# Kernel tuning notes

Hardware: AMD Instinct MI355X
Metric: run time of the kernel (lower is better)

Reference implementation:

```python
import jax, jax.numpy as jnp
import numpy as np


def setup_inputs() -> dict:
    key = jax.random.key(0)
    k1, k2 = jax.random.split(key)
    B, La, Lb, D = 32, 512, 512, 768
    a_bar = jax.random.normal(k1, (B, La, D), dtype=jnp.float32)
    b_bar = jax.random.normal(k2, (B, Lb, D), dtype=jnp.float32)
    return {"a_bar": a_bar, "b_bar": b_bar}


def reference(a_bar, b_bar):
    # e: [B, La, Lb] cross-attention scores
    e = jnp.einsum('bad,bcd->bac', a_bar, b_bar)
    # attend over b positions (softmax dim=2) -> aligned representation of a
    a_tilde = jnp.einsum('bac,bcd->bad', jax.nn.softmax(e, axis=2), b_bar)
    # attend over a positions (softmax dim=1), transpose, bmm with a_bar
    b_tilde = jnp.einsum('bac,bad->bcd', jax.nn.softmax(e, axis=1), a_bar)
    m_a = jnp.concatenate([a_bar, a_tilde, a_bar - a_tilde, a_bar * a_tilde], axis=-1)
    m_b = jnp.concatenate([b_bar, b_tilde, b_bar - b_tilde, b_bar * b_tilde], axis=-1)
    return (m_a, m_b)
```

## Files before the change

### kernel.cpp

```cpp
#include <hip/hip_runtime.h>
#include <hip/hip_bf16.h>
#include <math.h>

#define NB 32
#define LA 512
#define LB 512
#define DD 768

typedef __bf16 bf16x4 __attribute__((ext_vector_type(4)));
typedef __bf16 bf16x8 __attribute__((ext_vector_type(8)));
typedef float f32x4 __attribute__((ext_vector_type(4)));

__device__ __forceinline__ void gload_lds16(const void* g, void* l) {
  __builtin_amdgcn_global_load_lds(
      (const __attribute__((address_space(1))) unsigned int*)g,
      (__attribute__((address_space(3))) unsigned int*)l, 16, 0, 0);
}

__global__ __launch_bounds__(256) void convert_kernel(
    const float* __restrict__ A, const float* __restrict__ B,
    __bf16* __restrict__ Ah, __bf16* __restrict__ Al,
    __bf16* __restrict__ Bh, __bf16* __restrict__ Bl,
    __bf16* __restrict__ AhT, __bf16* __restrict__ BhT) {
  const int zb = blockIdx.z;
  const int b = zb & (NB - 1);
  const bool isB = zb >= NB;
  const float* src = (isB ? B : A) + (size_t)b * 512 * DD;
  __bf16* H = (isB ? Bh : Ah) + (size_t)b * 512 * DD;
  __bf16* L = (isB ? Bl : Al) + (size_t)b * 512 * DD;
  __bf16* T = (isB ? BhT : AhT) + (size_t)b * DD * 512;
  const int d0 = blockIdx.x * 64, i0 = blockIdx.y * 64;
  __shared__ __bf16 Tt[64][72];
  const int t = threadIdx.x;
  const int c4 = t & 15, r = t >> 4;
#pragma unroll
  for (int p = 0; p < 4; ++p) {
    const int i = i0 + r + p * 16;
    const float4 v = *(const float4*)(src + (size_t)i * DD + d0 + c4 * 4);
    float vv[4] = {v.x, v.y, v.z, v.w};
    bf16x4 h, l;
#pragma unroll
    for (int q = 0; q < 4; ++q) {
      h[q] = (__bf16)vv[q];
      l[q] = (__bf16)(vv[q] - (float)h[q]);
    }
    *(bf16x4*)(H + (size_t)i * DD + d0 + c4 * 4) = h;
    *(bf16x4*)(L + (size_t)i * DD + d0 + c4 * 4) = l;
#pragma unroll
    for (int q = 0; q < 4; ++q) Tt[c4 * 4 + q][r + p * 16] = h[q];
  }
  __syncthreads();
  const int cc = t & 7, rr = t >> 3;
#pragma unroll
  for (int p = 0; p < 2; ++p) {
    const int d = d0 + rr + p * 32;
    *(bf16x8*)(T + (size_t)d * 512 + i0 + cc * 8) =
        *(bf16x8*)&Tt[rr + p * 32][cc * 8];
  }
}

__global__ __launch_bounds__(256) void gemm_e_mfma(
    const __bf16* __restrict__ Ah, const __bf16* __restrict__ Al,
    const __bf16* __restrict__ Bh, const __bf16* __restrict__ Bl,
    float* __restrict__ E) {
  __shared__ __bf16 S[2][4][128][32];

  const int id = blockIdx.x;
  const int wg = (id & 7) * 64 + (id >> 3);
  const int b = wg >> 4, tl = wg & 15;
  const int i0 = (tl & 3) * 128, j0 = (tl >> 2) * 128;

  const __bf16* AhB = Ah + (size_t)b * LA * DD;
  const __bf16* AlB = Al + (size_t)b * LA * DD;
  const __bf16* BhB = Bh + (size_t)b * LB * DD;
  const __bf16* BlB = Bl + (size_t)b * LB * DD;
  float* Eb = E + (size_t)b * LA * LB;

  const int t = threadIdx.x;
  const int lane = t & 63, wave = t >> 6;
  const int wm = (wave >> 1) * 64, wn = (wave & 1) * 64;
  const int quad = lane >> 4, l16 = lane & 15;
  const int lrow = lane >> 2, lcol = (lane & 3) * 8;

  auto stage = [&](int buf, int k0) {
#pragma unroll
    for (int n = 0; n < 2; ++n) {
      const int c = n * 4 + wave;
      const int row = c * 16 + lrow;
      const size_t gA = (size_t)(i0 + row) * DD + k0 + lcol;
      const size_t gB = (size_t)(j0 + row) * DD + k0 + lcol;
      char* base = (char*)&S[buf][0][0][0];
      gload_lds16(AhB + gA, base + c * 1024);
      gload_lds16(AlB + gA, base + 8192 + c * 1024);
      gload_lds16(BhB + gB, base + 16384 + c * 1024);
      gload_lds16(BlB + gB, base + 24576 + c * 1024);
    }
  };

  f32x4 acc[4][4] = {};

  stage(0, 0);
  __syncthreads();
  int cur = 0;
  for (int k0 = 0; k0 < DD; k0 += 32) {
    if (k0 + 32 < DD) stage(cur ^ 1, k0 + 32);

    bf16x8 fah[4], fal[4], fbh[4], fbl[4];
#pragma unroll
    for (int f = 0; f < 4; ++f) {
      fah[f] = *(bf16x8*)&S[cur][0][wm + f * 16 + l16][quad * 8];
      fal[f] = *(bf16x8*)&S[cur][1][wm + f * 16 + l16][quad * 8];
      fbh[f] = *(bf16x8*)&S[cur][2][wn + f * 16 + l16][quad * 8];
      fbl[f] = *(bf16x8*)&S[cur][3][wn + f * 16 + l16][quad * 8];
    }
#pragma unroll
    for (int fm = 0; fm < 4; ++fm)
#pragma unroll
      for (int fn = 0; fn < 4; ++fn) {
        acc[fm][fn] = __builtin_amdgcn_mfma_f32_16x16x32_bf16(fah[fm], fbh[fn], acc[fm][fn], 0, 0, 0);
        acc[fm][fn] = __builtin_amdgcn_mfma_f32_16x16x32_bf16(fah[fm], fbl[fn], acc[fm][fn], 0, 0, 0);
        acc[fm][fn] = __builtin_amdgcn_mfma_f32_16x16x32_bf16(fal[fm], fbh[fn], acc[fm][fn], 0, 0, 0);
      }
    __syncthreads();
    cur ^= 1;
  }

#pragma unroll
  for (int fm = 0; fm < 4; ++fm)
#pragma unroll
    for (int r = 0; r < 4; ++r) {
      const int i = i0 + wm + fm * 16 + quad * 4 + r;
#pragma unroll
      for (int fn = 0; fn < 4; ++fn)
        Eb[(size_t)i * LB + j0 + wn + fn * 16 + l16] = acc[fm][fn][r];
    }
}

__global__ __launch_bounds__(256) void row_stats_kernel(
    const float* __restrict__ E, float* __restrict__ rmax,
    float* __restrict__ rsum) {
  const int wave = threadIdx.x >> 6;
  const int lane = threadIdx.x & 63;
  const int row = blockIdx.x * 4 + wave;
  const float* Er = E + (size_t)row * LB;
  float vals[8];
  float m = -INFINITY;
#pragma unroll
  for (int c = 0; c < 8; ++c) {
    vals[c] = Er[lane + c * 64];
    m = fmaxf(m, vals[c]);
  }
#pragma unroll
  for (int off = 32; off > 0; off >>= 1) m = fmaxf(m, __shfl_xor(m, off));
  float s = 0.f;
#pragma unroll
  for (int c = 0; c < 8; ++c) s += __expf(vals[c] - m);
#pragma unroll
  for (int off = 32; off > 0; off >>= 1) s += __shfl_xor(s, off);
  if (lane == 0) { rmax[row] = m; rsum[row] = s; }
}

__global__ __launch_bounds__(256) void col_partial(
    const float* __restrict__ E, float* __restrict__ pcm,
    float* __restrict__ pcs) {
  const int c = blockIdx.x * 256 + threadIdx.x;
  const int b = c >> 9, j = c & (LB - 1);
  const int i0 = blockIdx.y * 64;
  const float* Ep = E + ((size_t)b * LA + i0) * LB + j;
  float m = -INFINITY, s = 0.f;
#pragma unroll 4
  for (int i = 0; i < 64; ++i) {
    const float v = Ep[(size_t)i * LB];
    const float mn = fmaxf(m, v);
    s = s * __expf(m - mn) + __expf(v - mn);
    m = mn;
  }
  pcm[blockIdx.y * (NB * LB) + c] = m;
  pcs[blockIdx.y * (NB * LB) + c] = s;
}

__global__ __launch_bounds__(256) void col_combine(
    const float* __restrict__ pcm, const float* __restrict__ pcs,
    float* __restrict__ cmax, float* __restrict__ csum) {
  const int c = blockIdx.x * 256 + threadIdx.x;
  float m = -INFINITY, s = 0.f;
#pragma unroll
  for (int p = 0; p < 8; ++p) {
    const float mp = pcm[p * (NB * LB) + c];
    const float sp = pcs[p * (NB * LB) + c];
    const float mn = fmaxf(m, mp);
    s = s * __expf(m - mn) + sp * __expf(mp - mn);
    m = mn;
  }
  cmax[c] = m;
  csum[c] = s;
}

__global__ __launch_bounds__(256) void pconvert(
    const float* __restrict__ E, const float* __restrict__ rmax,
    const float* __restrict__ rsum, const float* __restrict__ cmax,
    const float* __restrict__ csum, __bf16* __restrict__ Pa,
    __bf16* __restrict__ PbT) {
  const int b = blockIdx.z;
  const int i0 = blockIdx.x * 128, j0 = blockIdx.y * 128;
  const float* Eb = E + (size_t)b * LA * LB;
  __shared__ __bf16 T[128][136];

  const int t = threadIdx.x;
  const int jr = t & 31, ir = t >> 5;
  const float4 cm4 = *(const float4*)&cmax[b * LB + j0 + jr * 4];
  const float4 cs4 = *(const float4*)&csum[b * LB + j0 + jr * 4];
  const float cmv[4] = {cm4.x, cm4.y, cm4.z, cm4.w};
  const float csv[4] = {1.f / cs4.x, 1.f / cs4.y, 1.f / cs4.z, 1.f / cs4.w};

#pragma unroll
  for (int p = 0; p < 16; ++p) {
    const int i = i0 + ir + p * 8;
    const float rm = rmax[b * LA + i];
    const float rs = 1.f / rsum[b * LA + i];
    const float4 v4 = *(const float4*)(Eb + (size_t)i * LB + j0 + jr * 4);
    const float v[4] = {v4.x, v4.y, v4.z, v4.w};
    bf16x4 pa;
#pragma unroll
    for (int q = 0; q < 4; ++q) {
      pa[q] = (__bf16)(__expf(v[q] - rm) * rs);
      T[jr * 4 + q][ir + p * 8] = (__bf16)(__expf(v[q] - cmv[q]) * csv[q]);
    }
    *(bf16x4*)(Pa + ((size_t)b * LA + i) * LB + j0 + jr * 4) = pa;
  }
  __syncthreads();
  const int jl = t >> 4, ch = t & 15;
#pragma unroll
  for (int p = 0; p < 8; ++p) {
    const int j = jl + p * 16;
    *(bf16x8*)(PbT + ((size_t)b * LB + j0 + j) * LA + i0 + ch * 8) =
        *(bf16x8*)&T[j][ch * 8];
  }
}

__global__ __launch_bounds__(256) void gemm_pd(
    const __bf16* __restrict__ P, const __bf16* __restrict__ T,
    const float* __restrict__ S, float* __restrict__ Mout) {
  __shared__ __bf16 Ls[2][2][128][32];

  const int id = blockIdx.x;
  const int wg = (id & 7) * 96 + (id >> 3);
  const int b = wg / 24, r24 = wg % 24;
  const int m0 = (r24 / 6) * 128, d0 = (r24 % 6) * 128;

  const __bf16* Pb = P + (size_t)b * 512 * 512;
  const __bf16* Tb = T + (size_t)b * DD * 512;
  const float* Sb = S + (size_t)b * 512 * DD;

  const int t = threadIdx.x;
  const int lane = t & 63, wave = t >> 6;
  const int wm = (wave >> 1) * 64, wn = (wave & 1) * 64;
  const int quad = lane >> 4, l16 = lane & 15;
  const int lrow = lane >> 2, lcol = (lane & 3) * 8;

  auto stage = [&](int buf, int k0) {
#pragma unroll
    for (int n = 0; n < 2; ++n) {
      const int c = n * 4 + wave;
      const int row = c * 16 + lrow;
      char* base = (char*)&Ls[buf][0][0][0];
      gload_lds16(Pb + (size_t)(m0 + row) * 512 + k0 + lcol, base + c * 1024);
      gload_lds16(Tb + (size_t)(d0 + row) * 512 + k0 + lcol,
                  base + 8192 + c * 1024);
    }
  };

  f32x4 acc[4][4] = {};

  stage(0, 0);
  __syncthreads();
  int cur = 0;
  for (int k0 = 0; k0 < 512; k0 += 32) {
    if (k0 + 32 < 512) stage(cur ^ 1, k0 + 32);

    bf16x8 fa[4], fb[4];
#pragma unroll
    for (int f = 0; f < 4; ++f) {
      fa[f] = *(bf16x8*)&Ls[cur][0][wm + f * 16 + l16][quad * 8];
      fb[f] = *(bf16x8*)&Ls[cur][1][wn + f * 16 + l16][quad * 8];
    }
#pragma unroll
    for (int fm = 0; fm < 4; ++fm)
#pragma unroll
      for (int fn = 0; fn < 4; ++fn)
        acc[fm][fn] = __builtin_amdgcn_mfma_f32_16x16x32_bf16(fa[fm], fb[fn], acc[fm][fn], 0, 0, 0);
    __syncthreads();
    cur ^= 1;
  }

#pragma unroll
  for (int fm = 0; fm < 4; ++fm)
#pragma unroll
    for (int r = 0; r < 4; ++r) {
      const int m = m0 + wm + fm * 16 + quad * 4 + r;
      float* base = Mout + ((size_t)b * 512 + m) * (4 * DD);
      const float* srow = Sb + (size_t)m * DD;
#pragma unroll
      for (int fn = 0; fn < 4; ++fn) {
        const int d = d0 + wn + fn * 16 + l16;
        const float sv = srow[d];
        const float tv = acc[fm][fn][r];
        base[d] = sv;
        base[DD + d] = tv;
        base[2 * DD + d] = sv - tv;
        base[3 * DD + d] = sv * tv;
      }
    }
}

extern "C" void kernel_launch(void* const* d_in, const int* in_sizes, int n_in,
                              void* d_out, int out_size, void* d_ws,
                              size_t ws_size, hipStream_t stream) {
  const float* a = (const float*)d_in[0];
  const float* bb = (const float*)d_in[1];
  float* out = (float*)d_out;
  float* Ma = out;
  float* Mb = out + (size_t)NB * LA * 4 * DD;

  char* p = (char*)d_ws;
  float* E = (float*)p;      p += (size_t)NB * LA * LB * 4;
  float* rmax = (float*)p;   p += (size_t)NB * LA * 4;
  float* rsum = (float*)p;   p += (size_t)NB * LA * 4;
  float* cmax = (float*)p;   p += (size_t)NB * LB * 4;
  float* csum = (float*)p;   p += (size_t)NB * LB * 4;
  float* pcm = (float*)p;    p += (size_t)8 * NB * LB * 4;
  float* pcs = (float*)p;    p += (size_t)8 * NB * LB * 4;
  __bf16* Ah = (__bf16*)p;   p += (size_t)NB * LA * DD * 2;
  __bf16* Al = (__bf16*)p;   p += (size_t)NB * LA * DD * 2;
  __bf16* Bh = (__bf16*)p;   p += (size_t)NB * LB * DD * 2;
  __bf16* Bl = (__bf16*)p;   p += (size_t)NB * LB * DD * 2;
  __bf16* AhT = (__bf16*)p;  p += (size_t)NB * DD * LA * 2;
  __bf16* BhT = (__bf16*)p;  p += (size_t)NB * DD * LB * 2;
  __bf16* Pa = (__bf16*)p;   p += (size_t)NB * LA * LB * 2;
  __bf16* PbT = (__bf16*)p;  p += (size_t)NB * LB * LA * 2;

  convert_kernel<<<dim3(DD / 64, 512 / 64, 2 * NB), 256, 0, stream>>>(
      a, bb, Ah, Al, Bh, Bl, AhT, BhT);
  gemm_e_mfma<<<dim3(512), 256, 0, stream>>>(Ah, Al, Bh, Bl, E);
  row_stats_kernel<<<dim3(NB * LA / 4), 256, 0, stream>>>(E, rmax, rsum);
  col_partial<<<dim3(NB * LB / 256, 8), 256, 0, stream>>>(E, pcm, pcs);
  col_combine<<<dim3(NB * LB / 256), 256, 0, stream>>>(pcm, pcs, cmax, csum);
  pconvert<<<dim3(LA / 128, LB / 128, NB), 256, 0, stream>>>(E, rmax, rsum,
                                                             cmax, csum, Pa, PbT);
  gemm_pd<<<dim3(768), 256, 0, stream>>>(Pa, BhT, a, Ma);
  gemm_pd<<<dim3(768), 256, 0, stream>>>(PbT, AhT, bb, Mb);
}
```

Baseline: 672.7 us.

## Fuse row/column softmax stats kernels and merge both output GEMMs into one launch

Merges the row-stats and column-partial kernels into one slab-based kernel that reads each 32-row slab of E for both row max/sum and per-column partial stats, with 16 slabs feeding col_combine. Both gemm_pd launches become a single 1536-block launch that picks the a-side or b-side operands by block index. Launch bounds with occupancy hints are added to the two GEMMs. The aim is to cut launch overhead and repeated E reads and to improve GPU fill. The risks are the smaller estat grid (512 blocks with serial per-wave row loops) and register pressure from the occupancy hints.

```diff
diff --git a/kernel.cpp b/kernel.cpp
--- a/kernel.cpp
+++ b/kernel.cpp
@@ -6,6 +6,7 @@
 #define LA 512
 #define LB 512
 #define DD 768
+#define SLABS 16
 
 typedef __bf16 bf16x4 __attribute__((ext_vector_type(4)));
 typedef __bf16 bf16x8 __attribute__((ext_vector_type(8)));
@@ -59,7 +60,7 @@
   }
 }
 
-__global__ __launch_bounds__(256) void gemm_e_mfma(
+__global__ __launch_bounds__(256, 2) void gemm_e_mfma(
     const __bf16* __restrict__ Ah, const __bf16* __restrict__ Al,
     const __bf16* __restrict__ Bh, const __bf16* __restrict__ Bl,
     float* __restrict__ E) {
@@ -136,47 +137,51 @@
     }
 }
 
-__global__ __launch_bounds__(256) void row_stats_kernel(
+__global__ __launch_bounds__(256) void estat_kernel(
     const float* __restrict__ E, float* __restrict__ rmax,
-    float* __restrict__ rsum) {
-  const int wave = threadIdx.x >> 6;
-  const int lane = threadIdx.x & 63;
-  const int row = blockIdx.x * 4 + wave;
-  const float* Er = E + (size_t)row * LB;
-  float vals[8];
-  float m = -INFINITY;
-#pragma unroll
-  for (int c = 0; c < 8; ++c) {
-    vals[c] = Er[lane + c * 64];
-    m = fmaxf(m, vals[c]);
-  }
-#pragma unroll
-  for (int off = 32; off > 0; off >>= 1) m = fmaxf(m, __shfl_xor(m, off));
-  float s = 0.f;
-#pragma unroll
-  for (int c = 0; c < 8; ++c) s += __expf(vals[c] - m);
-#pragma unroll
-  for (int off = 32; off > 0; off >>= 1) s += __shfl_xor(s, off);
-  if (lane == 0) { rmax[row] = m; rsum[row] = s; }
-}
-
-__global__ __launch_bounds__(256) void col_partial(
-    const float* __restrict__ E, float* __restrict__ pcm,
+    float* __restrict__ rsum, float* __restrict__ pcm,
     float* __restrict__ pcs) {
-  const int c = blockIdx.x * 256 + threadIdx.x;
-  const int b = c >> 9, j = c & (LB - 1);
-  const int i0 = blockIdx.y * 64;
-  const float* Ep = E + ((size_t)b * LA + i0) * LB + j;
-  float m = -INFINITY, s = 0.f;
+  const int b = blockIdx.x >> 4, slab = blockIdx.x & 15;
+  const int i0 = slab * 32;
+  const float* Eb = E + (size_t)b * LA * LB;
+  const int t = threadIdx.x;
+  const int wave = t >> 6, lane = t & 63;
+
+  for (int rr = 0; rr < 8; ++rr) {
+    const int i = i0 + wave * 8 + rr;
+    const float* Er = Eb + (size_t)i * LB;
+    float vals[8];
+    float m = -INFINITY;
+#pragma unroll
+    for (int c = 0; c < 8; ++c) {
+      vals[c] = Er[lane + c * 64];
+      m = fmaxf(m, vals[c]);
+    }
+#pragma unroll
+    for (int off = 32; off > 0; off >>= 1) m = fmaxf(m, __shfl_xor(m, off));
+    float s = 0.f;
+#pragma unroll
+    for (int c = 0; c < 8; ++c) s += __expf(vals[c] - m);
+#pragma unroll
+    for (int off = 32; off > 0; off >>= 1) s += __shfl_xor(s, off);
+    if (lane == 0) { rmax[b * LA + i] = m; rsum[b * LA + i] = s; }
+  }
+
+#pragma unroll
+  for (int h = 0; h < 2; ++h) {
+    const int j = t + h * 256;
+    const float* Ep = Eb + (size_t)i0 * LB + j;
+    float m = -INFINITY, s = 0.f;
 #pragma unroll 4
-  for (int i = 0; i < 64; ++i) {
-    const float v = Ep[(size_t)i * LB];
-    const float mn = fmaxf(m, v);
-    s = s * __expf(m - mn) + __expf(v - mn);
-    m = mn;
-  }
-  pcm[blockIdx.y * (NB * LB) + c] = m;
-  pcs[blockIdx.y * (NB * LB) + c] = s;
+    for (int i = 0; i < 32; ++i) {
+      const float v = Ep[(size_t)i * LB];
+      const float mn = fmaxf(m, v);
+      s = s * __expf(m - mn) + __expf(v - mn);
+      m = mn;
+    }
+    pcm[slab * (NB * LB) + b * LB + j] = m;
+    pcs[slab * (NB * LB) + b * LB + j] = s;
+  }
 }
 
 __global__ __launch_bounds__(256) void col_combine(
@@ -185,7 +190,7 @@
   const int c = blockIdx.x * 256 + threadIdx.x;
   float m = -INFINITY, s = 0.f;
 #pragma unroll
-  for (int p = 0; p < 8; ++p) {
+  for (int p = 0; p < SLABS; ++p) {
     const float mp = pcm[p * (NB * LB) + c];
     const float sp = pcs[p * (NB * LB) + c];
     const float mn = fmaxf(m, mp);
@@ -238,15 +243,24 @@
   }
 }
 
-__global__ __launch_bounds__(256) void gemm_pd(
-    const __bf16* __restrict__ P, const __bf16* __restrict__ T,
-    const float* __restrict__ S, float* __restrict__ Mout) {
+__global__ __launch_bounds__(256, 3) void gemm_pd(
+    const __bf16* __restrict__ Pa, const __bf16* __restrict__ BhT,
+    const float* __restrict__ A, float* __restrict__ Ma,
+    const __bf16* __restrict__ PbT, const __bf16* __restrict__ AhT,
+    const float* __restrict__ B, float* __restrict__ Mb) {
   __shared__ __bf16 Ls[2][2][128][32];
 
   const int id = blockIdx.x;
-  const int wg = (id & 7) * 96 + (id >> 3);
-  const int b = wg / 24, r24 = wg % 24;
+  const int wg = (id & 7) * 192 + (id >> 3);
+  const bool bside = wg >= 768;
+  const int wg2 = bside ? wg - 768 : wg;
+  const int b = wg2 / 24, r24 = wg2 % 24;
   const int m0 = (r24 / 6) * 128, d0 = (r24 % 6) * 128;
+
+  const __bf16* P = bside ? PbT : Pa;
+  const __bf16* T = bside ? AhT : BhT;
+  const float* S = bside ? B : A;
+  float* Mout = bside ? Mb : Ma;
 
   const __bf16* Pb = P + (size_t)b * 512 * 512;
   const __bf16* Tb = T + (size_t)b * DD * 512;
@@ -328,8 +342,8 @@
   float* rsum = (float*)p;   p += (size_t)NB * LA * 4;
   float* cmax = (float*)p;   p += (size_t)NB * LB * 4;
   float* csum = (float*)p;   p += (size_t)NB * LB * 4;
-  float* pcm = (float*)p;    p += (size_t)8 * NB * LB * 4;
-  float* pcs = (float*)p;    p += (size_t)8 * NB * LB * 4;
+  float* pcm = (float*)p;    p += (size_t)SLABS * NB * LB * 4;
+  float* pcs = (float*)p;    p += (size_t)SLABS * NB * LB * 4;
   __bf16* Ah = (__bf16*)p;   p += (size_t)NB * LA * DD * 2;
   __bf16* Al = (__bf16*)p;   p += (size_t)NB * LA * DD * 2;
   __bf16* Bh = (__bf16*)p;   p += (size_t)NB * LB * DD * 2;
@@ -342,11 +356,9 @@
   convert_kernel<<<dim3(DD / 64, 512 / 64, 2 * NB), 256, 0, stream>>>(
       a, bb, Ah, Al, Bh, Bl, AhT, BhT);
   gemm_e_mfma<<<dim3(512), 256, 0, stream>>>(Ah, Al, Bh, Bl, E);
-  row_stats_kernel<<<dim3(NB * LA / 4), 256, 0, stream>>>(E, rmax, rsum);
-  col_partial<<<dim3(NB * LB / 256, 8), 256, 0, stream>>>(E, pcm, pcs);
+  estat_kernel<<<dim3(NB * SLABS), 256, 0, stream>>>(E, rmax, rsum, pcm, pcs);
   col_combine<<<dim3(NB * LB / 256), 256, 0, stream>>>(pcm, pcs, cmax, csum);
   pconvert<<<dim3(LA / 128, LB / 128, NB), 256, 0, stream>>>(E, rmax, rsum,
                                                              cmax, csum, Pa, PbT);
-  gemm_pd<<<dim3(768), 256, 0, stream>>>(Pa, BhT, a, Ma);
-  gemm_pd<<<dim3(768), 256, 0, stream>>>(PbT, AhT, bb, Mb);
-}
+  gemm_pd<<<dim3(1536), 256, 0, stream>>>(Pa, BhT, a, Ma, PbT, AhT, bb, Mb);
+}
```

New measurement: 658.9 us. 1.02x faster.
